# Kernel tuning notes

Measured on AMD Instinct MI355X. Metric: run time of the kernel, lower is better.

## Reference

```python
import jax, jax.numpy as jnp
import numpy as np

D_MODEL, N_HEADS, N_AGENTS = 1024, 16, 64
HEAD_DIM = D_MODEL // N_HEADS
B, N = 4, 4096


def setup_inputs() -> dict:
    key = jax.random.key(0)
    ks = jax.random.split(key, 12)
    hs = HEAD_DIM
    inp = {
        "q": jax.random.normal(ks[0], (B, N_HEADS, N, hs), jnp.float32),
        "k": jax.random.normal(ks[1], (B, N_HEADS, N, hs), jnp.float32),
        "v": jax.random.normal(ks[2], (B, N_HEADS, N, hs), jnp.float32),
        # per-head linear layers (torch nn.Linear: y = x @ W.T + b)
        "Wq": jax.random.normal(ks[3], (hs, hs), jnp.float32) / np.sqrt(hs),
        "bq": jnp.zeros((hs,), jnp.float32),
        "Wk": jax.random.normal(ks[4], (hs, hs), jnp.float32) / np.sqrt(hs),
        "bk": jnp.zeros((hs,), jnp.float32),
        "Wv": jax.random.normal(ks[5], (hs, hs), jnp.float32) / np.sqrt(hs),
        "bv": jnp.zeros((hs,), jnp.float32),
        "Wo": jax.random.normal(ks[6], (D_MODEL, D_MODEL), jnp.float32) / np.sqrt(D_MODEL),
        "bo": jnp.zeros((D_MODEL,), jnp.float32),
        "agent_tokens": jax.random.normal(ks[7], (1, N_HEADS, N_AGENTS, hs), jnp.float32),
    }
    return inp


def reference(q, k, v, Wq, bq, Wk, bk, Wv, bv, Wo, bo, agent_tokens):
    Bq, nh, N_, hs = q.shape
    scale = 1.0 / np.sqrt(hs).astype(np.float32)
    agents = jnp.broadcast_to(agent_tokens, (Bq, nh, N_AGENTS, hs))
    q_agents = jnp.einsum("bhad,ed->bhae", agents, Wq) + bq   # [B,nh,A,hs]
    k_agents = jnp.einsum("bhnd,ed->bhne", k, Wk) + bk        # [B,nh,N,hs]
    v_agents = jnp.einsum("bhnd,ed->bhne", v, Wv) + bv        # [B,nh,N,hs]
    # stage 1: agents attend to keys/values
    scores1 = jnp.einsum("bhad,bhnd->bhan", q_agents, k_agents) * scale
    scores1 = jax.nn.softmax(scores1, axis=-1)
    context1 = jnp.einsum("bhan,bhnd->bhad", scores1, v_agents)  # [B,nh,A,hs]
    # stage 2: queries attend to agent context
    scores2 = jnp.einsum("bhnd,bhad->bhna", q, context1) * scale
    scores2 = jax.nn.softmax(scores2, axis=-1)
    context2 = jnp.einsum("bhna,bhad->bhnd", scores2, context1)  # [B,nh,N,hs]
    context2 = context2.transpose(0, 2, 1, 3).reshape(Bq, N_, nh * hs)
    output = context2 @ Wo.T + bo  # dropout is identity in eval
    return output, scores2
```

## Files before the change

### kernel.cpp

```cpp
#include <hip/hip_runtime.h>

#define NB 4
#define NH 16
#define NN 4096
#define HS 64
#define NA 64
#define DM 1024
#define NBH (NB*NH)
#define SCALE 0.125f

typedef __attribute__((ext_vector_type(8))) short bf16x8;
typedef __attribute__((ext_vector_type(4))) float f32x4;

__device__ __forceinline__ unsigned short f2bf(float f) {
  unsigned u = __float_as_uint(f);
  u += 0x7FFF + ((u >> 16) & 1);
  return (unsigned short)(u >> 16);
}

__device__ __forceinline__ void gload_lds16(const void* g, void* l) {
  __builtin_amdgcn_global_load_lds(
      (const __attribute__((address_space(1))) unsigned int*)g,
      (__attribute__((address_space(3))) unsigned int*)l, 16, 0, 0);
}

__device__ __forceinline__ void dot44(float (&c)[4][4], const float4 (&a)[4], const float4 (&b)[4]) {
#pragma unroll
  for (int i = 0; i < 4; ++i)
#pragma unroll
    for (int j = 0; j < 4; ++j) {
      c[i][j] = fmaf(a[i].x, b[j].x, c[i][j]);
      c[i][j] = fmaf(a[i].y, b[j].y, c[i][j]);
      c[i][j] = fmaf(a[i].z, b[j].z, c[i][j]);
      c[i][j] = fmaf(a[i].w, b[j].w, c[i][j]);
    }
}

__global__ __launch_bounds__(256) void k0_fold(
    const float* __restrict__ agents, const float* __restrict__ Wq,
    const float* __restrict__ bq, const float* __restrict__ Wk,
    unsigned short* __restrict__ foldqbf) {
  const int h = blockIdx.x, tid = threadIdx.x;
  const int tn = tid & 15, tm = tid >> 4;
  __shared__ float AG[64][68];
  __shared__ float WB[64][68];
  __shared__ float QA[64][68];
  __shared__ float WKT[64][68];
  for (int i = tid; i < 1024; i += 256) {
    const int r = i >> 4, c4 = (i & 15) * 4;
    *(float4*)&AG[r][c4] = *(const float4*)(agents + h * 4096 + r * 64 + c4);
    *(float4*)&WB[r][c4] = *(const float4*)(Wq + r * 64 + c4);
    const float4 f = *(const float4*)(Wk + r * 64 + c4);
    WKT[c4 + 0][r] = f.x; WKT[c4 + 1][r] = f.y;
    WKT[c4 + 2][r] = f.z; WKT[c4 + 3][r] = f.w;
  }
  __syncthreads();
  {
    const float4 bb = *(const float4*)(bq + tn * 4);
    float acc[4][4];
#pragma unroll
    for (int i = 0; i < 4; ++i) {
      acc[i][0] = bb.x; acc[i][1] = bb.y; acc[i][2] = bb.z; acc[i][3] = bb.w;
    }
    for (int d4 = 0; d4 < 64; d4 += 4) {
      float4 a4[4], b4[4];
#pragma unroll
      for (int i = 0; i < 4; ++i) a4[i] = *(const float4*)&AG[tm * 4 + i][d4];
#pragma unroll
      for (int j = 0; j < 4; ++j) b4[j] = *(const float4*)&WB[tn * 4 + j][d4];
      dot44(acc, a4, b4);
    }
#pragma unroll
    for (int i = 0; i < 4; ++i)
      *(float4*)&QA[tm * 4 + i][tn * 4] =
          make_float4(acc[i][0], acc[i][1], acc[i][2], acc[i][3]);
  }
  __syncthreads();
  {
    float acc[4][4] = {};
    for (int e4 = 0; e4 < 64; e4 += 4) {
      float4 a4[4], b4[4];
#pragma unroll
      for (int i = 0; i < 4; ++i) a4[i] = *(const float4*)&QA[tm * 4 + i][e4];
#pragma unroll
      for (int j = 0; j < 4; ++j) b4[j] = *(const float4*)&WKT[tn * 4 + j][e4];
      dot44(acc, a4, b4);
    }
#pragma unroll
    for (int i = 0; i < 4; ++i) {
      ushort4 o;
      o.x = f2bf(acc[i][0] * SCALE); o.y = f2bf(acc[i][1] * SCALE);
      o.z = f2bf(acc[i][2] * SCALE); o.w = f2bf(acc[i][3] * SCALE);
      *(ushort4*)(foldqbf + h * 4096 + (tm * 4 + i) * 64 + tn * 4) = o;
    }
  }
}

__global__ __launch_bounds__(256) void k2_mfma(
    const float* __restrict__ kraw, const float* __restrict__ vraw,
    const unsigned short* __restrict__ foldqbf,
    float* __restrict__ pctx, float* __restrict__ psum) {
  __shared__ unsigned short FQ[64 * 72];
  __shared__ unsigned short KN[64 * 72];
  __shared__ unsigned short VT[64 * 72];
  __shared__ unsigned short ES[64 * 72];
  const int chunk = blockIdx.x, bh = blockIdx.y, h = bh & 15;
  const int tid = threadIdx.x;
  const int lane = tid & 63, w = tid >> 6;
  const int l15 = lane & 15, lg = lane >> 4;

  const size_t kvbase = ((size_t)bh * NN + chunk * 256) * HS;
  float4 kreg[4], vreg[4];
#pragma unroll
  for (int i0 = 0; i0 < 4; ++i0) {
    const int i = tid + i0 * 256;
    kreg[i0] = *(const float4*)(kraw + kvbase + (size_t)i * 4);
    vreg[i0] = *(const float4*)(vraw + kvbase + (size_t)i * 4);
  }

  for (int i = tid; i < 512; i += 256) {
    const int a = i >> 3, d8 = (i & 7) * 8;
    *(uint4*)&FQ[a * 72 + d8] = *(const uint4*)(foldqbf + h * 4096 + a * 64 + d8);
  }

  f32x4 ctx[4];
#pragma unroll
  for (int df = 0; df < 4; ++df) ctx[df] = (f32x4){0.f, 0.f, 0.f, 0.f};
  f32x4 pacc = (f32x4){0.f, 0.f, 0.f, 0.f};
  const short one_bf = (short)0x3F80;
  const bf16x8 ones = {one_bf, one_bf, one_bf, one_bf, one_bf, one_bf, one_bf, one_bf};

  for (int t = 0; t < 4; ++t) {
    __syncthreads();
#pragma unroll
    for (int i0 = 0; i0 < 4; ++i0) {
      const int i = tid + i0 * 256;
      const int n = i >> 4, d4 = (i & 15) * 4;
      const float4 f = kreg[i0];
      const unsigned klo = f2bf(f.x) | ((unsigned)f2bf(f.y) << 16);
      const unsigned khi = f2bf(f.z) | ((unsigned)f2bf(f.w) << 16);
      *(uint2*)&KN[n * 72 + d4] = make_uint2(klo, khi);
      const float4 g = vreg[i0];
      const int nn = n ^ (8 * (i & 7));
      VT[(d4 + 0) * 72 + nn] = f2bf(g.x);
      VT[(d4 + 1) * 72 + nn] = f2bf(g.y);
      VT[(d4 + 2) * 72 + nn] = f2bf(g.z);
      VT[(d4 + 3) * 72 + nn] = f2bf(g.w);
    }
    if (t < 3) {
#pragma unroll
      for (int i0 = 0; i0 < 4; ++i0) {
        const int i = tid + i0 * 256;
        kreg[i0] = *(const float4*)(kraw + kvbase + (size_t)(t + 1) * 4096 + (size_t)i * 4);
        vreg[i0] = *(const float4*)(vraw + kvbase + (size_t)(t + 1) * 4096 + (size_t)i * 4);
      }
    }
    __syncthreads();
    const bf16x8 bq0 = *(const bf16x8*)&FQ[(w * 16 + l15) * 72 + lg * 8];
    const bf16x8 bq1 = *(const bf16x8*)&FQ[(w * 16 + l15) * 72 + 32 + lg * 8];
    f32x4 sacc[4];
#pragma unroll
    for (int nf = 0; nf < 4; ++nf) {
      sacc[nf] = (f32x4){0.f, 0.f, 0.f, 0.f};
      const bf16x8 a0 = *(const bf16x8*)&KN[(nf * 16 + l15) * 72 + lg * 8];
      const bf16x8 a1 = *(const bf16x8*)&KN[(nf * 16 + l15) * 72 + 32 + lg * 8];
      sacc[nf] = __builtin_amdgcn_mfma_f32_16x16x32_bf16(a0, bq0, sacc[nf], 0, 0, 0);
      sacc[nf] = __builtin_amdgcn_mfma_f32_16x16x32_bf16(a1, bq1, sacc[nf], 0, 0, 0);
    }
#pragma unroll
    for (int nf = 0; nf < 4; ++nf) {
      const unsigned e0 = f2bf(__expf(sacc[nf][0])) | ((unsigned)f2bf(__expf(sacc[nf][1])) << 16);
      const unsigned e1 = f2bf(__expf(sacc[nf][2])) | ((unsigned)f2bf(__expf(sacc[nf][3])) << 16);
      *(uint2*)&ES[(w * 16 + l15) * 72 + nf * 16 + lg * 4] = make_uint2(e0, e1);
    }
    const bf16x8 ea0 = *(const bf16x8*)&ES[(w * 16 + l15) * 72 + lg * 8];
    const bf16x8 ea1 = *(const bf16x8*)&ES[(w * 16 + l15) * 72 + 32 + lg * 8];
    pacc = __builtin_amdgcn_mfma_f32_16x16x32_bf16(ea0, ones, pacc, 0, 0, 0);
    pacc = __builtin_amdgcn_mfma_f32_16x16x32_bf16(ea1, ones, pacc, 0, 0, 0);
#pragma unroll
    for (int df = 0; df < 4; ++df) {
      const int d = df * 16 + l15;
      const int sw = 8 * ((d >> 2) & 7);
      const bf16x8 vb0 = *(const bf16x8*)&VT[d * 72 + ((lg * 8) ^ sw)];
      const bf16x8 vb1 = *(const bf16x8*)&VT[d * 72 + ((32 + lg * 8) ^ sw)];
      ctx[df] = __builtin_amdgcn_mfma_f32_16x16x32_bf16(ea0, vb0, ctx[df], 0, 0, 0);
      ctx[df] = __builtin_amdgcn_mfma_f32_16x16x32_bf16(ea1, vb1, ctx[df], 0, 0, 0);
    }
  }
  const size_t pbase = ((size_t)bh * 16 + chunk) * 4096;
#pragma unroll
  for (int df = 0; df < 4; ++df)
#pragma unroll
    for (int r = 0; r < 4; ++r)
      pctx[pbase + (w * 16 + lg * 4 + r) * 64 + df * 16 + l15] = ctx[df][r];
  if (l15 == 0) {
#pragma unroll
    for (int r = 0; r < 4; ++r)
      psum[((size_t)bh * 16 + chunk) * 64 + w * 16 + lg * 4 + r] = pacc[r];
  }
}

__global__ __launch_bounds__(256) void k3_reduce(
    const float* __restrict__ pctx, const float* __restrict__ psum,
    const float* __restrict__ Wv, const float* __restrict__ bv,
    unsigned short* __restrict__ c1nbf) {
  const int bh = blockIdx.x, aq = blockIdx.y;
  const int tid = threadIdx.x;
  const int tn = tid & 15, tm = tid >> 4;
  __shared__ float sinv[16];
  __shared__ float CR[16][68];
  __shared__ float WT[64][68];
  if (tid < 16) {
    const int a = aq * 16 + tid;
    float s = 0.f;
#pragma unroll 4
    for (int c = 0; c < 16; ++c) s += psum[((size_t)bh * 16 + c) * 64 + a];
    sinv[tid] = 1.0f / s;
  }
  for (int i = tid; i < 1024; i += 256) {
    const int e = i >> 4, d4 = (i & 15) * 4;
    const float4 f = *(const float4*)(Wv + e * 64 + d4);
    WT[d4 + 0][e] = f.x; WT[d4 + 1][e] = f.y;
    WT[d4 + 2][e] = f.z; WT[d4 + 3][e] = f.w;
  }
  __syncthreads();
  {
    const int al = tid >> 4, d4 = (tid & 15) * 4;
    const size_t base = (size_t)bh * 16 * 4096 + (size_t)(aq * 16 + al) * 64 + d4;
    float4 s = make_float4(0.f, 0.f, 0.f, 0.f);
#pragma unroll 4
    for (int c = 0; c < 16; ++c) {
      const float4 f = *(const float4*)(pctx + base + (size_t)c * 4096);
      s.x += f.x; s.y += f.y; s.z += f.z; s.w += f.w;
    }
    const float si = sinv[al];
    CR[al][d4 + 0] = s.x * si; CR[al][d4 + 1] = s.y * si;
    CR[al][d4 + 2] = s.z * si; CR[al][d4 + 3] = s.w * si;
  }
  __syncthreads();
  float acc[4];
  const float4 bb = *(const float4*)(bv + tn * 4);
  acc[0] = bb.x; acc[1] = bb.y; acc[2] = bb.z; acc[3] = bb.w;
#pragma unroll 8
  for (int d = 0; d < 64; ++d) {
    const float a0 = CR[tm][d];
    const float4 wv4 = *(const float4*)&WT[d][tn * 4];
    acc[0] = fmaf(a0, wv4.x, acc[0]);
    acc[1] = fmaf(a0, wv4.y, acc[1]);
    acc[2] = fmaf(a0, wv4.z, acc[2]);
    acc[3] = fmaf(a0, wv4.w, acc[3]);
  }
  ushort4 o;
  o.x = f2bf(acc[0]); o.y = f2bf(acc[1]); o.z = f2bf(acc[2]); o.w = f2bf(acc[3]);
  *(ushort4*)(c1nbf + (size_t)bh * 4096 + (size_t)(aq * 16 + tm) * 64 + tn * 4) = o;
}

__global__ __launch_bounds__(256) void kG(
    const unsigned short* __restrict__ c1nbf, const float* __restrict__ Wo,
    unsigned short* __restrict__ GT) {
  const int et = blockIdx.x;
  const int bh = blockIdx.y, h = bh & 15;
  const int e0 = et * 256;
  __shared__ unsigned short WoS[256 * 72];
  __shared__ unsigned short C1S[64 * 72];
  const int tid = threadIdx.x;
  const int lane = tid & 63, w = tid >> 6;
  const int l15 = lane & 15, lg = lane >> 4;
  for (int i = tid; i < 4096; i += 256) {
    const int e = i >> 4, d4 = (i & 15) * 4;
    const float4 f = *(const float4*)(Wo + (size_t)(e0 + e) * DM + h * 64 + d4);
    ushort4 o;
    o.x = f2bf(f.x); o.y = f2bf(f.y); o.z = f2bf(f.z); o.w = f2bf(f.w);
    *(ushort4*)&WoS[e * 72 + d4] = o;
  }
  for (int i = tid; i < 512; i += 256) {
    const int a = i >> 3, d8 = (i & 7) * 8;
    *(uint4*)&C1S[a * 72 + d8] =
        *(const uint4*)(c1nbf + (size_t)bh * 4096 + a * 64 + d8);
  }
  __syncthreads();
  bf16x8 b0[4], b1[4];
#pragma unroll
  for (int at = 0; at < 4; ++at) {
    b0[at] = *(const bf16x8*)&C1S[(at * 16 + l15) * 72 + lg * 8];
    b1[at] = *(const bf16x8*)&C1S[(at * 16 + l15) * 72 + 32 + lg * 8];
  }
#pragma unroll
  for (int et16 = 0; et16 < 4; ++et16) {
    const int erow = w * 64 + et16 * 16 + l15;
    const bf16x8 a0 = *(const bf16x8*)&WoS[erow * 72 + lg * 8];
    const bf16x8 a1 = *(const bf16x8*)&WoS[erow * 72 + 32 + lg * 8];
#pragma unroll
    for (int at = 0; at < 4; ++at) {
      f32x4 acc = (f32x4){0.f, 0.f, 0.f, 0.f};
      acc = __builtin_amdgcn_mfma_f32_16x16x32_bf16(a0, b0[at], acc, 0, 0, 0);
      acc = __builtin_amdgcn_mfma_f32_16x16x32_bf16(a1, b1[at], acc, 0, 0, 0);
      const size_t gbase =
          ((size_t)bh * 1024 + e0 + w * 64 + et16 * 16 + lg * 4) * 64 + at * 16 + l15;
#pragma unroll
      for (int r = 0; r < 4; ++r) GT[gbase + (size_t)r * 64] = f2bf(acc[r]);
    }
  }
}

__global__ __launch_bounds__(256) void k4_mfma(
    const float* __restrict__ q, const unsigned short* __restrict__ c1nbf,
    float* __restrict__ scores2, unsigned short* __restrict__ P2bf) {
  __shared__ unsigned short C1N[64 * 72];
  __shared__ unsigned short PS[64 * 72];
  const int bh = blockIdx.y;
  const int n0 = blockIdx.x * 64;
  const int tid = threadIdx.x;
  const int lane = tid & 63, w = tid >> 6;
  const int l15 = lane & 15, lg = lane >> 4;

  for (int i = tid; i < 512; i += 256) {
    const int a = i >> 3, d8 = (i & 7) * 8;
    *(uint4*)&C1N[a * 72 + d8] =
        *(const uint4*)(c1nbf + (size_t)bh * 4096 + a * 64 + d8);
  }
  const float* qr = q + ((size_t)bh * NN + n0 + w * 16 + l15) * HS;
  const float4 qa = *(const float4*)(qr + lg * 8);
  const float4 qb = *(const float4*)(qr + lg * 8 + 4);
  const float4 qc = *(const float4*)(qr + 32 + lg * 8);
  const float4 qd = *(const float4*)(qr + 32 + lg * 8 + 4);
  bf16x8 af0, af1;
  af0[0] = (short)f2bf(qa.x * SCALE); af0[1] = (short)f2bf(qa.y * SCALE);
  af0[2] = (short)f2bf(qa.z * SCALE); af0[3] = (short)f2bf(qa.w * SCALE);
  af0[4] = (short)f2bf(qb.x * SCALE); af0[5] = (short)f2bf(qb.y * SCALE);
  af0[6] = (short)f2bf(qb.z * SCALE); af0[7] = (short)f2bf(qb.w * SCALE);
  af1[0] = (short)f2bf(qc.x * SCALE); af1[1] = (short)f2bf(qc.y * SCALE);
  af1[2] = (short)f2bf(qc.z * SCALE); af1[3] = (short)f2bf(qc.w * SCALE);
  af1[4] = (short)f2bf(qd.x * SCALE); af1[5] = (short)f2bf(qd.y * SCALE);
  af1[6] = (short)f2bf(qd.z * SCALE); af1[7] = (short)f2bf(qd.w * SCALE);
  __syncthreads();

  f32x4 sacc[4];
#pragma unroll
  for (int afr = 0; afr < 4; ++afr) {
    sacc[afr] = (f32x4){0.f, 0.f, 0.f, 0.f};
    const bf16x8 b0 = *(const bf16x8*)&C1N[(afr * 16 + l15) * 72 + lg * 8];
    const bf16x8 b1 = *(const bf16x8*)&C1N[(afr * 16 + l15) * 72 + 32 + lg * 8];
    sacc[afr] = __builtin_amdgcn_mfma_f32_16x16x32_bf16(af0, b0, sacc[afr], 0, 0, 0);
    sacc[afr] = __builtin_amdgcn_mfma_f32_16x16x32_bf16(af1, b1, sacc[afr], 0, 0, 0);
  }
  float p[4][4];
#pragma unroll
  for (int r = 0; r < 4; ++r) {
    float m = fmaxf(fmaxf(sacc[0][r], sacc[1][r]), fmaxf(sacc[2][r], sacc[3][r]));
#pragma unroll
    for (int off = 1; off < 16; off <<= 1) m = fmaxf(m, __shfl_xor(m, off));
    float s = 0.f;
#pragma unroll
    for (int afr = 0; afr < 4; ++afr) {
      p[afr][r] = __expf(sacc[afr][r] - m);
      s += p[afr][r];
    }
#pragma unroll
    for (int off = 1; off < 16; off <<= 1) s += __shfl_xor(s, off);
    const float inv = 1.0f / s;
    const size_t srow = ((size_t)bh * NN + n0 + w * 16 + lg * 4 + r) * NA;
#pragma unroll
    for (int afr = 0; afr < 4; ++afr) {
      p[afr][r] *= inv;
      scores2[srow + afr * 16 + l15] = p[afr][r];
      PS[(w * 16 + lg * 4 + r) * 72 + afr * 16 + l15] = f2bf(p[afr][r]);
    }
  }
  const int prow = w * 16 + (lane >> 2);
  const int pch = (lane & 3) * 16;
  const uint4 v0 = *(const uint4*)&PS[prow * 72 + pch];
  const uint4 v1 = *(const uint4*)&PS[prow * 72 + pch + 8];
  unsigned short* gp = P2bf + ((size_t)bh * NN + n0 + prow) * NA + pch;
  *(uint4*)gp = v0;
  *(uint4*)(gp + 8) = v1;
}

__global__ __launch_bounds__(512, 4) void k5_mfma(
    const unsigned short* __restrict__ P2, const unsigned short* __restrict__ GT,
    const float* __restrict__ bo, float* __restrict__ out) {
  __shared__ unsigned short As[256 * 64];
  __shared__ unsigned short Bs[128 * 64];
  const int tid = threadIdx.x;
  const int lane = tid & 63;
  const int w = tid >> 6;
  const int wr = w >> 2, wc = w & 3;
  const int l15 = lane & 15, lg = lane >> 4;
  const int rp = blockIdx.x;
  const int e0 = blockIdx.y * 128;
  const int b16 = (rp >> 4) * 16;
  const int nloc0 = (rp & 15) * 256;

  const int srow8 = lane >> 3;
  const int sslot = ((lane & 7) ^ srow8) << 4;

  f32x4 acc[8][2] = {{{0.f}}};

  for (int t = 0; t < 16; ++t) {
    const char* Ab = (const char*)(P2 + ((size_t)(b16 + t) * NN + nloc0) * NA);
    const char* Gb = (const char*)(GT + ((size_t)(b16 + t) * 1024 + e0) * NA);
#pragma unroll
    for (int j = 0; j < 4; ++j) {
      const int rb = j * 64 + w * 8;
      gload_lds16(Ab + (size_t)(rb + srow8) * 128 + sslot,
                  (char*)As + rb * 128 + lane * 16);
    }
#pragma unroll
    for (int j = 0; j < 2; ++j) {
      const int rb = j * 64 + w * 8;
      gload_lds16(Gb + (size_t)(rb + srow8) * 128 + sslot,
                  (char*)Bs + rb * 128 + lane * 16);
    }
    __syncthreads();
#pragma unroll
    for (int ks = 0; ks < 2; ++ks) {
      bf16x8 af[8], bfr[2];
#pragma unroll
      for (int m = 0; m < 8; ++m) {
        const int r = wr * 128 + m * 16 + l15;
        const int byt = (ks * 64 + lg * 16) ^ ((r & 7) << 4);
        af[m] = *(const bf16x8*)((const char*)As + r * 128 + byt);
      }
#pragma unroll
      for (int n = 0; n < 2; ++n) {
        const int r = wc * 32 + n * 16 + l15;
        const int byt = (ks * 64 + lg * 16) ^ ((r & 7) << 4);
        bfr[n] = *(const bf16x8*)((const char*)Bs + r * 128 + byt);
      }
#pragma unroll
      for (int m = 0; m < 8; ++m)
#pragma unroll
        for (int n = 0; n < 2; ++n)
          acc[m][n] = __builtin_amdgcn_mfma_f32_16x16x32_bf16(af[m], bfr[n], acc[m][n], 0, 0, 0);
    }
    __syncthreads();
  }

  const size_t mrow0 = (size_t)(b16 >> 4) * NN + nloc0;
#pragma unroll
  for (int m = 0; m < 8; ++m) {
    const size_t row0 = mrow0 + wr * 128 + m * 16 + lg * 4;
#pragma unroll
    for (int n = 0; n < 2; ++n) {
      const int c = e0 + wc * 32 + n * 16 + l15;
      const float bias = bo[c];
#pragma unroll
      for (int r = 0; r < 4; ++r)
        out[(row0 + r) * DM + c] = acc[m][n][r] + bias;
    }
  }
}

extern "C" void kernel_launch(void* const* d_in, const int* in_sizes, int n_in,
                              void* d_out, int out_size, void* d_ws, size_t ws_size,
                              hipStream_t stream) {
  (void)in_sizes; (void)n_in; (void)out_size; (void)ws_size;
  const float* q  = (const float*)d_in[0];
  const float* k  = (const float*)d_in[1];
  const float* v  = (const float*)d_in[2];
  const float* Wq = (const float*)d_in[3];
  const float* bq = (const float*)d_in[4];
  const float* Wk = (const float*)d_in[5];
  const float* bk = (const float*)d_in[6];
  const float* Wv = (const float*)d_in[7];
  const float* bv = (const float*)d_in[8];
  const float* Wo = (const float*)d_in[9];
  const float* bo = (const float*)d_in[10];
  const float* ag = (const float*)d_in[11];
  (void)bk;

  float* out0 = (float*)d_out;
  float* scores2 = out0 + (size_t)NB * NN * DM;

  float* ws = (float*)d_ws;
  unsigned short* foldqbf = (unsigned short*)ws;
  unsigned short* c1nbf = (unsigned short*)(ws + 65536);
  float* psum = ws + 65536 + 262144;
  float* pctx = psum + 65536;
  unsigned short* GT = (unsigned short*)pctx;
  unsigned short* P2bf = (unsigned short*)(pctx + 4194304);

  k0_fold<<<NH, 256, 0, stream>>>(ag, Wq, bq, Wk, foldqbf);
  k2_mfma<<<dim3(16, NBH), 256, 0, stream>>>(k, v, foldqbf, pctx, psum);
  k3_reduce<<<dim3(NBH, 4), 256, 0, stream>>>(pctx, psum, Wv, bv, c1nbf);
  kG<<<dim3(4, NBH), 256, 0, stream>>>(c1nbf, Wo, GT);
  k4_mfma<<<dim3(NN / 64, NBH), 256, 0, stream>>>(q, c1nbf, scores2, P2bf);
  k5_mfma<<<dim3(64, 8), 512, 0, stream>>>(P2bf, GT, bo, out0);
}
```

Before: 141.9 us.

## Drop bf16 probability copy; convert fp32 scores2 to bf16 inside output GEMM

```diff
diff --git a/kernel.cpp b/kernel.cpp
--- a/kernel.cpp
+++ b/kernel.cpp
@@ -16,6 +16,12 @@
   unsigned u = __float_as_uint(f);
   u += 0x7FFF + ((u >> 16) & 1);
   return (unsigned short)(u >> 16);
+}
+
+__device__ __forceinline__ unsigned pk2bf(float lo, float hi) {
+  unsigned r;
+  asm("v_cvt_pk_bf16_f32 %0, %1, %2" : "=v"(r) : "v"(lo), "v"(hi));
+  return r;
 }
 
 __device__ __forceinline__ void gload_lds16(const void* g, void* l) {
@@ -305,9 +311,8 @@
 
 __global__ __launch_bounds__(256) void k4_mfma(
     const float* __restrict__ q, const unsigned short* __restrict__ c1nbf,
-    float* __restrict__ scores2, unsigned short* __restrict__ P2bf) {
+    float* __restrict__ scores2) {
   __shared__ unsigned short C1N[64 * 72];
-  __shared__ unsigned short PS[64 * 72];
   const int bh = blockIdx.y;
   const int n0 = blockIdx.x * 64;
   const int tid = threadIdx.x;
@@ -344,40 +349,30 @@
     sacc[afr] = __builtin_amdgcn_mfma_f32_16x16x32_bf16(af0, b0, sacc[afr], 0, 0, 0);
     sacc[afr] = __builtin_amdgcn_mfma_f32_16x16x32_bf16(af1, b1, sacc[afr], 0, 0, 0);
   }
-  float p[4][4];
 #pragma unroll
   for (int r = 0; r < 4; ++r) {
     float m = fmaxf(fmaxf(sacc[0][r], sacc[1][r]), fmaxf(sacc[2][r], sacc[3][r]));
 #pragma unroll
     for (int off = 1; off < 16; off <<= 1) m = fmaxf(m, __shfl_xor(m, off));
+    float p[4];
     float s = 0.f;
 #pragma unroll
     for (int afr = 0; afr < 4; ++afr) {
-      p[afr][r] = __expf(sacc[afr][r] - m);
-      s += p[afr][r];
+      p[afr] = __expf(sacc[afr][r] - m);
+      s += p[afr];
     }
 #pragma unroll
     for (int off = 1; off < 16; off <<= 1) s += __shfl_xor(s, off);
     const float inv = 1.0f / s;
     const size_t srow = ((size_t)bh * NN + n0 + w * 16 + lg * 4 + r) * NA;
 #pragma unroll
-    for (int afr = 0; afr < 4; ++afr) {
-      p[afr][r] *= inv;
-      scores2[srow + afr * 16 + l15] = p[afr][r];
-      PS[(w * 16 + lg * 4 + r) * 72 + afr * 16 + l15] = f2bf(p[afr][r]);
-    }
-  }
-  const int prow = w * 16 + (lane >> 2);
-  const int pch = (lane & 3) * 16;
-  const uint4 v0 = *(const uint4*)&PS[prow * 72 + pch];
-  const uint4 v1 = *(const uint4*)&PS[prow * 72 + pch + 8];
-  unsigned short* gp = P2bf + ((size_t)bh * NN + n0 + prow) * NA + pch;
-  *(uint4*)gp = v0;
-  *(uint4*)(gp + 8) = v1;
+    for (int afr = 0; afr < 4; ++afr)
+      scores2[srow + afr * 16 + l15] = p[afr] * inv;
+  }
 }
 
 __global__ __launch_bounds__(512, 4) void k5_mfma(
-    const unsigned short* __restrict__ P2, const unsigned short* __restrict__ GT,
+    const float* __restrict__ S2, const unsigned short* __restrict__ GT,
     const float* __restrict__ bo, float* __restrict__ out) {
   __shared__ unsigned short As[256 * 64];
   __shared__ unsigned short Bs[128 * 64];
@@ -393,23 +388,34 @@
 
   const int srow8 = lane >> 3;
   const int sslot = ((lane & 7) ^ srow8) << 4;
+  const int arow = tid >> 1;
+  const int ahalf = tid & 1;
 
   f32x4 acc[8][2] = {{{0.f}}};
 
   for (int t = 0; t < 16; ++t) {
-    const char* Ab = (const char*)(P2 + ((size_t)(b16 + t) * NN + nloc0) * NA);
     const char* Gb = (const char*)(GT + ((size_t)(b16 + t) * 1024 + e0) * NA);
-#pragma unroll
-    for (int j = 0; j < 4; ++j) {
-      const int rb = j * 64 + w * 8;
-      gload_lds16(Ab + (size_t)(rb + srow8) * 128 + sslot,
-                  (char*)As + rb * 128 + lane * 16);
-    }
 #pragma unroll
     for (int j = 0; j < 2; ++j) {
       const int rb = j * 64 + w * 8;
       gload_lds16(Gb + (size_t)(rb + srow8) * 128 + sslot,
                   (char*)Bs + rb * 128 + lane * 16);
+    }
+    const float* Ar = S2 + ((size_t)(b16 + t) * NN + nloc0 + arow) * NA + ahalf * 32;
+#pragma unroll
+    for (int p = 0; p < 2; ++p) {
+      float4 fa[4];
+#pragma unroll
+      for (int j = 0; j < 4; ++j) fa[j] = *(const float4*)(Ar + p * 16 + j * 4);
+#pragma unroll
+      for (int j = 0; j < 2; ++j) {
+        const unsigned u0 = pk2bf(fa[2 * j].x, fa[2 * j].y);
+        const unsigned u1 = pk2bf(fa[2 * j].z, fa[2 * j].w);
+        const unsigned u2 = pk2bf(fa[2 * j + 1].x, fa[2 * j + 1].y);
+        const unsigned u3 = pk2bf(fa[2 * j + 1].z, fa[2 * j + 1].w);
+        const int byt = (ahalf * 64 + p * 32 + j * 16) ^ ((arow & 7) << 4);
+        *(uint4*)((char*)As + arow * 128 + byt) = make_uint4(u0, u1, u2, u3);
+      }
     }
     __syncthreads();
 #pragma unroll
@@ -478,12 +484,11 @@
   float* psum = ws + 65536 + 262144;
   float* pctx = psum + 65536;
   unsigned short* GT = (unsigned short*)pctx;
-  unsigned short* P2bf = (unsigned short*)(pctx + 4194304);
 
   k0_fold<<<NH, 256, 0, stream>>>(ag, Wq, bq, Wk, foldqbf);
   k2_mfma<<<dim3(16, NBH), 256, 0, stream>>>(k, v, foldqbf, pctx, psum);
   k3_reduce<<<dim3(NBH, 4), 256, 0, stream>>>(pctx, psum, Wv, bv, c1nbf);
   kG<<<dim3(4, NBH), 256, 0, stream>>>(c1nbf, Wo, GT);
-  k4_mfma<<<dim3(NN / 64, NBH), 256, 0, stream>>>(q, c1nbf, scores2, P2bf);
-  k5_mfma<<<dim3(64, 8), 512, 0, stream>>>(P2bf, GT, bo, out0);
-}
+  k4_mfma<<<dim3(NN / 64, NBH), 256, 0, stream>>>(q, c1nbf, scores2);
+  k5_mfma<<<dim3(64, 8), 512, 0, stream>>>(scores2, GT, bo, out0);
+}
```

After: 181.6 us. +28.0%, slower.
